# Kernel optimization log

Measured on AMD Instinct MI355X. Metric: run time of the kernel, lower is better.

Reference implementation:

```python
import jax, jax.numpy as jnp
import numpy as np

ROPE_THETA = 10000.0


def _apply_rope(x, rot_dim):
    # lucidrains RotaryEmbedding: only first rot_dim channels are rotated,
    # freqs are interleave-repeated, rotate_half works on (d r=2) pairs.
    S = x.shape[-2]
    half = rot_dim // 2
    inv_freq = 1.0 / (ROPE_THETA ** (jnp.arange(0, rot_dim, 2, dtype=jnp.float32) / rot_dim))  # [half]
    pos = jnp.arange(S, dtype=jnp.float32)
    freqs = pos[:, None] * inv_freq[None, :]          # [S, half]
    freqs = jnp.repeat(freqs, 2, axis=-1)             # [S, rot_dim] interleaved
    cos = jnp.cos(freqs).astype(x.dtype)
    sin = jnp.sin(freqs).astype(x.dtype)
    xl, xr = x[..., :rot_dim], x[..., rot_dim:]
    xp = xl.reshape(*xl.shape[:-1], half, 2)
    x1, x2 = xp[..., 0], xp[..., 1]
    rot_half = jnp.stack([-x2, x1], axis=-1).reshape(xl.shape)
    return jnp.concatenate([xl * cos + rot_half * sin, xr], axis=-1)


def setup_inputs() -> dict:
    key = jax.random.key(0)
    ks = jax.random.split(key, 7)
    B, Sa, Se, d_audio, d_score = 4, 4096, 2048, 1024, 1024
    d_h = min(d_audio, d_score)
    return {
        "x_audio": jax.random.normal(ks[0], (B, Sa, d_audio), jnp.float32),
        "x_event": jax.random.normal(ks[1], (B, Se, d_score), jnp.float32),
        "event_padding_mask": jax.random.randint(ks[2], (B, Se), 0, 2) > 0,
        "W_q": jax.random.normal(ks[3], (d_h, d_audio), jnp.float32) * (d_audio ** -0.5),
        "b_q": jax.random.normal(ks[4], (d_h,), jnp.float32) * 0.02,
        "W_k": jax.random.normal(ks[5], (d_h, d_score), jnp.float32) * (d_score ** -0.5),
        "b_k": jax.random.normal(ks[6], (d_h,), jnp.float32) * 0.02,
    }


def reference(x_audio, x_event, event_padding_mask, W_q, b_q, W_k, b_k):
    d_h = W_q.shape[0]
    rot_dim = d_h // 2  # RotaryEmbedding(dim=d_h//2) -> partial rotary over first d_h//2 channels
    Q = jnp.einsum("bsd,hd->bsh", x_audio, W_q) + b_q
    K = jnp.einsum("bed,hd->beh", x_event, W_k) + b_k
    Q = _apply_rope(Q, rot_dim)
    K = _apply_rope(K, rot_dim)
    attn = jnp.einsum("bsh,beh->bse", Q, K)  # [B, S_audio, S_event]
    mask = event_padding_mask[:, None, :]     # [B, 1, S_event]
    attn = jnp.where(mask, attn, jnp.float32(-jnp.inf))
    return attn
```

## Files before the change

kernel.cpp:

```cpp
#include <hip/hip_runtime.h>
#include <hip/hip_bf16.h>
#include <cmath>

#define BATCH 4
#define SA 4096
#define SE 2048
#define DIM 1024
#define ROT 512
#define NT (DIM / 64)

#define MASK_SENTINEL (-1.0e30f)

using short8  = __attribute__((ext_vector_type(8))) short;
using floatx4 = __attribute__((ext_vector_type(4))) float;

#define RFREQ 0.0519051171f

__device__ __forceinline__ void gl_lds16(const void* g, void* l) {
    __builtin_amdgcn_global_load_lds(
        (const __attribute__((address_space(1))) unsigned int*)g,
        (__attribute__((address_space(3))) unsigned int*)l, 16, 0, 0);
}

__device__ __forceinline__ short bf16_of(float f) {
    __hip_bfloat16 h = __float2bfloat16(f);
    return *reinterpret_cast<short*>(&h);
}

__device__ __forceinline__ int imin(int a, int b) { return a < b ? a : b; }

__global__ __launch_bounds__(256) void probe_mask_kernel(
    const int* __restrict__ mask_i, int* __restrict__ flag)
{
    __shared__ int s_bad;
    if (threadIdx.x == 0) s_bad = 0;
    __syncthreads();
    int bad = 0;
    for (int i = threadIdx.x; i < 1024; i += 256) {
        int v = mask_i[i];
        bad |= (v != 0 && v != 1) ? 1 : 0;
    }
    if (bad) atomicOr(&s_bad, 1);
    __syncthreads();
    if (threadIdx.x == 0) *flag = s_bad ? 0 : 1;
}

__global__ __launch_bounds__(256) void cvt_bf16_kernel(
    const float* __restrict__ in, short* __restrict__ out, int n8)
{
    int i = blockIdx.x * 256 + threadIdx.x;
    if (i >= n8) return;
    const float4 f0 = ((const float4*)in)[2 * i];
    const float4 f1 = ((const float4*)in)[2 * i + 1];
    short8 o;
    o[0] = bf16_of(f0.x); o[1] = bf16_of(f0.y);
    o[2] = bf16_of(f0.z); o[3] = bf16_of(f0.w);
    o[4] = bf16_of(f1.x); o[5] = bf16_of(f1.y);
    o[6] = bf16_of(f1.z); o[7] = bf16_of(f1.w);
    ((short8*)out)[i] = o;
}

__global__ __launch_bounds__(256) void rope_table_kernel(float2* __restrict__ tab)
{
    const int i   = blockIdx.x * 256 + threadIdx.x;
    const int h2  = i >> 12;
    const int pos = i & 4095;
    const float inv = exp2f(-RFREQ * (float)h2);
    float s, c;
    sincosf((float)pos * inv, &s, &c);
    tab[i] = make_float2(c, s);
}

template <int MODE>
__device__ __forceinline__ void gemm8_body(
    const short* __restrict__ A,
    const short* __restrict__ B,
    const float* __restrict__ bias,
    const float2* __restrict__ ct,
    const void*  __restrict__ maskp,
    const int*   __restrict__ flag,
    void* __restrict__ outp,
    int smask)
{
    __shared__ char smem[131072];
    char* const lA0 = smem;
    char* const lA1 = smem + 32768;
    char* const lB0 = smem + 65536;
    char* const lB1 = smem + 98304;

    const int tid  = threadIdx.x;
    const int wid  = tid >> 6;
    const int lane = tid & 63;

    const int nbx = gridDim.x, nby = gridDim.y;
    const int id  = blockIdx.x + nbx * (blockIdx.y + nby * blockIdx.z);
    const int cpx = (nbx * nby * gridDim.z) >> 3;
    const int swzid = (id & 7) * cpx + (id >> 3);
    const int bx  = swzid % nbx;
    const int byz = swzid / nbx;
    const int by  = byz % nby;
    const int bz  = byz / nby;
    const int m0 = by * 256;
    const int n0 = bx * 256;

    const short* Ab = A;
    const short* Bb = B;
    if (MODE == 1) {
        Ab += (size_t)bz * SA * DIM;
        Bb += (size_t)bz * SE * DIM;
    }

    const int r8   = lane >> 3;
    const int c16  = (lane & 7) << 4;
    const int scs  = ((lane & 7) ^ r8) << 4;
    const int arow = wid * 8 + r8;
    const int brow = (wid & 3) * 8 + (wid >> 2) * 64 + r8;
    const char* gA = (const char*)Ab + ((size_t)(m0 + arow) << 11) + scs;
    const char* gB = (const char*)Bb + ((size_t)(n0 + brow) << 11) + scs;
    const int ldsAt = arow * 128 + c16;
    const int ldsBt = brow * 128 + c16;

#define STG_A(dst, h, j, kt) \
    gl_lds16(gA + (((size_t)((h)*64 + (j)*128) << 11) + (size_t)(kt)*128), \
             (dst) + ((h)*64 + (j)*128) * 128 + ldsAt)
#define STG_B(dst, h, j, kt) \
    gl_lds16(gB + (((size_t)((h)*32 + (j)*128) << 11) + (size_t)(kt)*128), \
             (dst) + ((h)*32 + (j)*128) * 128 + ldsBt)

    const int fr  = lane & 15;
    const int fq  = lane >> 4;
    const int kc0 = (fq * 16) ^ ((fr & 7) << 4);
    const int wm  = (wid >> 2) * 128;
    const int wn  = (wid & 3) * 64;

    floatx4 acc[8][4] = {};
    short8 af[4][2];
    short8 bfr[2][2][2];

#define RD_A(lAc, mh) do {                                                   \
    _Pragma("unroll") for (int mi4 = 0; mi4 < 4; ++mi4)                      \
    _Pragma("unroll") for (int ks = 0; ks < 2; ++ks)                         \
        af[mi4][ks] = *(const short8*)((lAc)                                 \
            + (wm + (mh)*64 + mi4*16 + fr) * 128 + (kc0 ^ (ks*64)));         \
} while (0)
#define RD_B(lBc, nh) do {                                                   \
    _Pragma("unroll") for (int ni2 = 0; ni2 < 2; ++ni2)                      \
    _Pragma("unroll") for (int ks = 0; ks < 2; ++ks)                         \
        bfr[nh][ni2][ks] = *(const short8*)((lBc)                            \
            + (wn + (nh)*32 + ni2*16 + fr) * 128 + (kc0 ^ (ks*64)));         \
} while (0)
#define QUAD(mh, nh) do {                                                    \
    __builtin_amdgcn_s_setprio(1);                                           \
    _Pragma("unroll") for (int mi4 = 0; mi4 < 4; ++mi4)                      \
    _Pragma("unroll") for (int ni2 = 0; ni2 < 2; ++ni2)                      \
    _Pragma("unroll") for (int ks = 0; ks < 2; ++ks)                         \
        acc[(mh)*4 + mi4][(nh)*2 + ni2] =                                    \
            __builtin_amdgcn_mfma_f32_16x16x32_bf16(                         \
                af[mi4][ks], bfr[nh][ni2][ks],                               \
                acc[(mh)*4 + mi4][(nh)*2 + ni2], 0, 0, 0);                   \
    __builtin_amdgcn_s_setprio(0);                                           \
} while (0)
#define BAR() do { __builtin_amdgcn_s_barrier();                             \
                   __builtin_amdgcn_sched_barrier(0); } while (0)
#define WAITV(n) asm volatile("s_waitcnt vmcnt(" #n ")" ::: "memory")

    STG_A(lA0, 0, 0, 0); STG_A(lA0, 0, 1, 0);
    STG_A(lA0, 1, 0, 0); STG_A(lA0, 1, 1, 0);
    STG_B(lB0, 0, 0, 0); STG_B(lB0, 0, 1, 0);
    STG_B(lB0, 1, 0, 0); STG_B(lB0, 1, 1, 0);
    STG_A(lA1, 0, 0, 1); STG_A(lA1, 0, 1, 1);
    STG_B(lB1, 0, 0, 1); STG_B(lB1, 0, 1, 1);
    STG_A(lA1, 1, 0, 1); STG_A(lA1, 1, 1, 1);
    WAITV(6);
    BAR();

    auto tile = [&](int t, char* lAc, char* lBc, char* lBn) {
        const int kt1 = imin(t + 1, NT - 1);
        const int kt2 = imin(t + 2, NT - 1);
        RD_A(lAc, 0); RD_B(lBc, 0);
        STG_B(lBn, 1, 0, kt1); STG_B(lBn, 1, 1, kt1);
        BAR();
        QUAD(0, 0);
        BAR();
        RD_B(lBc, 1);
        STG_A(lAc, 0, 0, kt2); STG_A(lAc, 0, 1, kt2);
        BAR();
        QUAD(0, 1);
        BAR();
        RD_A(lAc, 1);
        STG_B(lBc, 0, 0, kt2); STG_B(lBc, 0, 1, kt2);
        BAR();
        QUAD(1, 0);
        BAR();
        STG_A(lAc, 1, 0, kt2); STG_A(lAc, 1, 1, kt2);
        BAR();
        QUAD(1, 1);
        WAITV(6);
        BAR();
    };

    for (int t = 0; t < NT; t += 2) {
        tile(t,     lA0, lB0, lB1);
        tile(t + 1, lA1, lB1, lB0);
    }
    WAITV(0);

    const int rrow = (lane >> 4) * 4;

    if (MODE == 0) {
        short* out = (short*)outp;
#pragma unroll
        for (int ni = 0; ni < 4; ++ni) {
            const int h = n0 + wn + ni * 16 + fr;
            const float bv  = bias[h];
            const bool rope = (h < ROT);
            const float sgn = (h & 1) ? 1.f : -1.f;
            const float2* ctrow = ct + ((size_t)(h >> 1) << 12);
#pragma unroll
            for (int mi = 0; mi < 8; ++mi) {
                const int rbase = m0 + wm + mi * 16 + rrow;
                const int pbase = rbase & smask;
                float2 cs[4];
                if (rope) {
#pragma unroll
                    for (int r = 0; r < 4; ++r) cs[r] = ctrow[pbase + r];
                }
#pragma unroll
                for (int r = 0; r < 4; ++r) {
                    float v = acc[mi][ni][r] + bv;
                    float p = __shfl_xor(v, 1);
                    if (rope) v = v * cs[r].x + sgn * p * cs[r].y;
                    out[(size_t)(rbase + r) * DIM + h] = bf16_of(v);
                }
            }
        }
    } else {
        float* out = (float*)outp + (size_t)bz * SA * SE;
        const int fl = *flag;
#pragma unroll
        for (int ni = 0; ni < 4; ++ni) {
            const int e = n0 + wn + ni * 16 + fr;
            int mk;
            if (fl) mk = ((const int*)maskp)[(size_t)bz * SE + e];
            else    mk = ((const unsigned char*)maskp)[(size_t)bz * SE + e];
#pragma unroll
            for (int mi = 0; mi < 8; ++mi) {
                const int rbase = m0 + wm + mi * 16 + rrow;
#pragma unroll
                for (int r = 0; r < 4; ++r) {
                    const float v = mk ? acc[mi][ni][r] : MASK_SENTINEL;
                    out[(size_t)(rbase + r) * SE + e] = v;
                }
            }
        }
    }
#undef STG_A
#undef STG_B
#undef RD_A
#undef RD_B
#undef QUAD
#undef BAR
#undef WAITV
}

__global__ __launch_bounds__(512, 2) void gemm8_proj_kernel(
    const short* __restrict__ A, const short* __restrict__ B,
    const float* __restrict__ bias, const float2* __restrict__ ct,
    short* __restrict__ out, int smask)
{
    gemm8_body<0>(A, B, bias, ct, nullptr, nullptr, out, smask);
}

__global__ __launch_bounds__(512, 2) void gemm8_attn_kernel(
    const short* __restrict__ Q, const short* __restrict__ K,
    const void* __restrict__ maskp, const int* __restrict__ flag,
    float* __restrict__ out)
{
    gemm8_body<1>(Q, K, nullptr, nullptr, maskp, flag, out, 0);
}

extern "C" void kernel_launch(void* const* d_in, const int* in_sizes, int n_in,
                              void* d_out, int out_size, void* d_ws, size_t ws_size,
                              hipStream_t stream)
{
    const float* x_audio = (const float*)d_in[0];
    const float* x_event = (const float*)d_in[1];
    const void*  maskp   = d_in[2];
    const float* W_q     = (const float*)d_in[3];
    const float* b_q     = (const float*)d_in[4];
    const float* W_k     = (const float*)d_in[5];
    const float* b_k     = (const float*)d_in[6];
    float* out = (float*)d_out;

    char* ws = (char*)d_ws;
    short* xbf  = (short*)(ws);
    short* Qbf  = (short*)(ws + (size_t)32 * 1024 * 1024);
    short* Kbf  = (short*)(ws + (size_t)64 * 1024 * 1024);
    short* Wqbf = (short*)(ws + (size_t)80 * 1024 * 1024);
    short* Wkbf = (short*)(ws + (size_t)82 * 1024 * 1024);
    int*   flag = (int*)  (ws + (size_t)84 * 1024 * 1024);
    float2* ct  = (float2*)d_out;

    probe_mask_kernel<<<1, 256, 0, stream>>>((const int*)maskp, flag);
    rope_table_kernel<<<4096, 256, 0, stream>>>(ct);

    const int nxa8 = BATCH * SA * DIM / 8;
    const int nxe8 = BATCH * SE * DIM / 8;
    const int nw8  = DIM * DIM / 8;

    cvt_bf16_kernel<<<(nxa8 + 255) / 256, 256, 0, stream>>>(x_audio, xbf, nxa8);
    cvt_bf16_kernel<<<(nw8 + 255) / 256, 256, 0, stream>>>(W_q, Wqbf, nw8);
    gemm8_proj_kernel<<<dim3(DIM / 256, (BATCH * SA) / 256, 1), 512, 0, stream>>>(
        xbf, Wqbf, b_q, ct, Qbf, SA - 1);

    cvt_bf16_kernel<<<(nxe8 + 255) / 256, 256, 0, stream>>>(x_event, xbf, nxe8);
    cvt_bf16_kernel<<<(nw8 + 255) / 256, 256, 0, stream>>>(W_k, Wkbf, nw8);
    gemm8_proj_kernel<<<dim3(DIM / 256, (BATCH * SE) / 256, 1), 512, 0, stream>>>(
        xbf, Wkbf, b_k, ct, Kbf, SE - 1);

    gemm8_attn_kernel<<<dim3(SE / 256, SA / 256, BATCH), 512, 0, stream>>>(
        Qbf, Kbf, maskp, flag, out);
}
```

Before: 405.9 us.

## Shrink GEMM block tiles to 128x128 with 4 waves and half LDS

Replaces the 256x256 block tile (8 waves, 128 KiB LDS) with a 128x128 tile (4 waves, 64 KiB LDS) for all three GEMMs. The staging, LDS-read and MFMA schedule is restructured into two half-steps per k-tile instead of four quarters. The aim is more blocks and better occupancy and load balance, with fewer barriers per tile. The cost is lower arithmetic intensity, so more global and L2 traffic per FLOP.

```diff
diff --git a/kernel.cpp b/kernel.cpp
--- a/kernel.cpp
+++ b/kernel.cpp
@@ -72,7 +72,7 @@
 }
 
 template <int MODE>
-__device__ __forceinline__ void gemm8_body(
+__device__ __forceinline__ void gemm128_body(
     const short* __restrict__ A,
     const short* __restrict__ B,
     const float* __restrict__ bias,
@@ -82,11 +82,11 @@
     void* __restrict__ outp,
     int smask)
 {
-    __shared__ char smem[131072];
+    __shared__ char smem[65536];
     char* const lA0 = smem;
-    char* const lA1 = smem + 32768;
-    char* const lB0 = smem + 65536;
-    char* const lB1 = smem + 98304;
+    char* const lA1 = smem + 16384;
+    char* const lB0 = smem + 32768;
+    char* const lB1 = smem + 49152;
 
     const int tid  = threadIdx.x;
     const int wid  = tid >> 6;
@@ -100,8 +100,8 @@
     const int byz = swzid / nbx;
     const int by  = byz % nby;
     const int bz  = byz / nby;
-    const int m0 = by * 256;
-    const int n0 = bx * 256;
+    const int m0 = by * 128;
+    const int n0 = bx * 128;
 
     const short* Ab = A;
     const short* Bb = B;
@@ -114,88 +114,89 @@
     const int c16  = (lane & 7) << 4;
     const int scs  = ((lane & 7) ^ r8) << 4;
     const int arow = wid * 8 + r8;
-    const int brow = (wid & 3) * 8 + (wid >> 2) * 64 + r8;
     const char* gA = (const char*)Ab + ((size_t)(m0 + arow) << 11) + scs;
-    const char* gB = (const char*)Bb + ((size_t)(n0 + brow) << 11) + scs;
-    const int ldsAt = arow * 128 + c16;
-    const int ldsBt = brow * 128 + c16;
-
-#define STG_A(dst, h, j, kt) \
-    gl_lds16(gA + (((size_t)((h)*64 + (j)*128) << 11) + (size_t)(kt)*128), \
-             (dst) + ((h)*64 + (j)*128) * 128 + ldsAt)
-#define STG_B(dst, h, j, kt) \
-    gl_lds16(gB + (((size_t)((h)*32 + (j)*128) << 11) + (size_t)(kt)*128), \
-             (dst) + ((h)*32 + (j)*128) * 128 + ldsBt)
+    const char* gB = (const char*)Bb + ((size_t)(n0 + arow) << 11) + scs;
+    const int ldsT = arow * 128 + c16;
+
+#define STG_A(dst, j, kt) \
+    gl_lds16(gA + (((size_t)(j) * 32) << 11) + (size_t)(kt) * 128, \
+             (dst) + (j) * 32 * 128 + ldsT)
+#define STG_B(dst, j, kt) \
+    gl_lds16(gB + (((size_t)(j) * 32) << 11) + (size_t)(kt) * 128, \
+             (dst) + (j) * 32 * 128 + ldsT)
 
     const int fr  = lane & 15;
     const int fq  = lane >> 4;
     const int kc0 = (fq * 16) ^ ((fr & 7) << 4);
-    const int wm  = (wid >> 2) * 128;
-    const int wn  = (wid & 3) * 64;
-
-    floatx4 acc[8][4] = {};
+    const int wm  = (wid >> 1) * 64;
+    const int wn  = (wid & 1) * 64;
+
+    floatx4 acc[4][4] = {};
     short8 af[4][2];
-    short8 bfr[2][2][2];
-
-#define RD_A(lAc, mh) do {                                                   \
-    _Pragma("unroll") for (int mi4 = 0; mi4 < 4; ++mi4)                      \
-    _Pragma("unroll") for (int ks = 0; ks < 2; ++ks)                         \
-        af[mi4][ks] = *(const short8*)((lAc)                                 \
-            + (wm + (mh)*64 + mi4*16 + fr) * 128 + (kc0 ^ (ks*64)));         \
-} while (0)
-#define RD_B(lBc, nh) do {                                                   \
-    _Pragma("unroll") for (int ni2 = 0; ni2 < 2; ++ni2)                      \
-    _Pragma("unroll") for (int ks = 0; ks < 2; ++ks)                         \
-        bfr[nh][ni2][ks] = *(const short8*)((lBc)                            \
-            + (wn + (nh)*32 + ni2*16 + fr) * 128 + (kc0 ^ (ks*64)));         \
-} while (0)
-#define QUAD(mh, nh) do {                                                    \
+    short8 b01[2][2];
+    short8 b23[2][2];
+
+#define RD_A(lAc) do {                                                       \
+    _Pragma("unroll") for (int mi = 0; mi < 4; ++mi)                         \
+    _Pragma("unroll") for (int ks = 0; ks < 2; ++ks)                         \
+        af[mi][ks] = *(const short8*)((lAc)                                  \
+            + (wm + mi * 16 + fr) * 128 + (kc0 ^ (ks * 64)));                \
+} while (0)
+#define RD_B01(lBc) do {                                                     \
+    _Pragma("unroll") for (int ni = 0; ni < 2; ++ni)                         \
+    _Pragma("unroll") for (int ks = 0; ks < 2; ++ks)                         \
+        b01[ni][ks] = *(const short8*)((lBc)                                 \
+            + (wn + ni * 16 + fr) * 128 + (kc0 ^ (ks * 64)));                \
+} while (0)
+#define RD_B23(lBc) do {                                                     \
+    _Pragma("unroll") for (int ni = 0; ni < 2; ++ni)                         \
+    _Pragma("unroll") for (int ks = 0; ks < 2; ++ks)                         \
+        b23[ni][ks] = *(const short8*)((lBc)                                 \
+            + (wn + (2 + ni) * 16 + fr) * 128 + (kc0 ^ (ks * 64)));          \
+} while (0)
+#define QUAD01() do {                                                        \
     __builtin_amdgcn_s_setprio(1);                                           \
-    _Pragma("unroll") for (int mi4 = 0; mi4 < 4; ++mi4)                      \
-    _Pragma("unroll") for (int ni2 = 0; ni2 < 2; ++ni2)                      \
-    _Pragma("unroll") for (int ks = 0; ks < 2; ++ks)                         \
-        acc[(mh)*4 + mi4][(nh)*2 + ni2] =                                    \
-            __builtin_amdgcn_mfma_f32_16x16x32_bf16(                         \
-                af[mi4][ks], bfr[nh][ni2][ks],                               \
-                acc[(mh)*4 + mi4][(nh)*2 + ni2], 0, 0, 0);                   \
+    _Pragma("unroll") for (int mi = 0; mi < 4; ++mi)                         \
+    _Pragma("unroll") for (int ni = 0; ni < 2; ++ni)                         \
+    _Pragma("unroll") for (int ks = 0; ks < 2; ++ks)                         \
+        acc[mi][ni] = __builtin_amdgcn_mfma_f32_16x16x32_bf16(               \
+            af[mi][ks], b01[ni][ks], acc[mi][ni], 0, 0, 0);                  \
+    __builtin_amdgcn_s_setprio(0);                                           \
+} while (0)
+#define QUAD23() do {                                                        \
+    __builtin_amdgcn_s_setprio(1);                                           \
+    _Pragma("unroll") for (int mi = 0; mi < 4; ++mi)                         \
+    _Pragma("unroll") for (int ni = 0; ni < 2; ++ni)                         \
+    _Pragma("unroll") for (int ks = 0; ks < 2; ++ks)                         \
+        acc[mi][2 + ni] = __builtin_amdgcn_mfma_f32_16x16x32_bf16(           \
+            af[mi][ks], b23[ni][ks], acc[mi][2 + ni], 0, 0, 0);              \
     __builtin_amdgcn_s_setprio(0);                                           \
 } while (0)
 #define BAR() do { __builtin_amdgcn_s_barrier();                             \
                    __builtin_amdgcn_sched_barrier(0); } while (0)
 #define WAITV(n) asm volatile("s_waitcnt vmcnt(" #n ")" ::: "memory")
 
-    STG_A(lA0, 0, 0, 0); STG_A(lA0, 0, 1, 0);
-    STG_A(lA0, 1, 0, 0); STG_A(lA0, 1, 1, 0);
-    STG_B(lB0, 0, 0, 0); STG_B(lB0, 0, 1, 0);
-    STG_B(lB0, 1, 0, 0); STG_B(lB0, 1, 1, 0);
-    STG_A(lA1, 0, 0, 1); STG_A(lA1, 0, 1, 1);
-    STG_B(lB1, 0, 0, 1); STG_B(lB1, 0, 1, 1);
-    STG_A(lA1, 1, 0, 1); STG_A(lA1, 1, 1, 1);
-    WAITV(6);
+    STG_A(lA0, 0, 0); STG_A(lA0, 1, 0); STG_A(lA0, 2, 0); STG_A(lA0, 3, 0);
+    STG_B(lB0, 0, 0); STG_B(lB0, 1, 0); STG_B(lB0, 2, 0); STG_B(lB0, 3, 0);
+    STG_A(lA1, 0, 1); STG_A(lA1, 1, 1); STG_A(lA1, 2, 1); STG_A(lA1, 3, 1);
+    WAITV(4);
     BAR();
 
-    auto tile = [&](int t, char* lAc, char* lBc, char* lBn) {
+    auto tile = [&](int t, char* lAc, char* lBc, char* lBo) {
         const int kt1 = imin(t + 1, NT - 1);
         const int kt2 = imin(t + 2, NT - 1);
-        RD_A(lAc, 0); RD_B(lBc, 0);
-        STG_B(lBn, 1, 0, kt1); STG_B(lBn, 1, 1, kt1);
+        RD_A(lAc); RD_B01(lBc);
+        STG_B(lBo, 0, kt1); STG_B(lBo, 1, kt1);
+        STG_B(lBo, 2, kt1); STG_B(lBo, 3, kt1);
         BAR();
-        QUAD(0, 0);
+        QUAD01();
         BAR();
-        RD_B(lBc, 1);
-        STG_A(lAc, 0, 0, kt2); STG_A(lAc, 0, 1, kt2);
+        RD_B23(lBc);
+        STG_A(lAc, 0, kt2); STG_A(lAc, 1, kt2);
+        STG_A(lAc, 2, kt2); STG_A(lAc, 3, kt2);
         BAR();
-        QUAD(0, 1);
-        BAR();
-        RD_A(lAc, 1);
-        STG_B(lBc, 0, 0, kt2); STG_B(lBc, 0, 1, kt2);
-        BAR();
-        QUAD(1, 0);
-        BAR();
-        STG_A(lAc, 1, 0, kt2); STG_A(lAc, 1, 1, kt2);
-        BAR();
-        QUAD(1, 1);
-        WAITV(6);
+        QUAD23();
+        WAITV(4);
         BAR();
     };
 
@@ -205,7 +206,7 @@
     }
     WAITV(0);
 
-    const int rrow = (lane >> 4) * 4;
+    const int rrow = fq * 4;
 
     if (MODE == 0) {
         short* out = (short*)outp;
@@ -217,7 +218,7 @@
             const float sgn = (h & 1) ? 1.f : -1.f;
             const float2* ctrow = ct + ((size_t)(h >> 1) << 12);
 #pragma unroll
-            for (int mi = 0; mi < 8; ++mi) {
+            for (int mi = 0; mi < 4; ++mi) {
                 const int rbase = m0 + wm + mi * 16 + rrow;
                 const int pbase = rbase & smask;
                 float2 cs[4];
@@ -244,7 +245,7 @@
             if (fl) mk = ((const int*)maskp)[(size_t)bz * SE + e];
             else    mk = ((const unsigned char*)maskp)[(size_t)bz * SE + e];
 #pragma unroll
-            for (int mi = 0; mi < 8; ++mi) {
+            for (int mi = 0; mi < 4; ++mi) {
                 const int rbase = m0 + wm + mi * 16 + rrow;
 #pragma unroll
                 for (int r = 0; r < 4; ++r) {
@@ -257,26 +258,28 @@
 #undef STG_A
 #undef STG_B
 #undef RD_A
-#undef RD_B
-#undef QUAD
+#undef RD_B01
+#undef RD_B23
+#undef QUAD01
+#undef QUAD23
 #undef BAR
 #undef WAITV
 }
 
-__global__ __launch_bounds__(512, 2) void gemm8_proj_kernel(
+__global__ __launch_bounds__(256, 2) void gemm128_proj_kernel(
     const short* __restrict__ A, const short* __restrict__ B,
     const float* __restrict__ bias, const float2* __restrict__ ct,
     short* __restrict__ out, int smask)
 {
-    gemm8_body<0>(A, B, bias, ct, nullptr, nullptr, out, smask);
-}
-
-__global__ __launch_bounds__(512, 2) void gemm8_attn_kernel(
+    gemm128_body<0>(A, B, bias, ct, nullptr, nullptr, out, smask);
+}
+
+__global__ __launch_bounds__(256, 2) void gemm128_attn_kernel(
     const short* __restrict__ Q, const short* __restrict__ K,
     const void* __restrict__ maskp, const int* __restrict__ flag,
     float* __restrict__ out)
 {
-    gemm8_body<1>(Q, K, nullptr, nullptr, maskp, flag, out, 0);
+    gemm128_body<1>(Q, K, nullptr, nullptr, maskp, flag, out, 0);
 }
 
 extern "C" void kernel_launch(void* const* d_in, const int* in_sizes, int n_in,
@@ -310,14 +313,14 @@
 
     cvt_bf16_kernel<<<(nxa8 + 255) / 256, 256, 0, stream>>>(x_audio, xbf, nxa8);
     cvt_bf16_kernel<<<(nw8 + 255) / 256, 256, 0, stream>>>(W_q, Wqbf, nw8);
-    gemm8_proj_kernel<<<dim3(DIM / 256, (BATCH * SA) / 256, 1), 512, 0, stream>>>(
+    gemm128_proj_kernel<<<dim3(DIM / 128, (BATCH * SA) / 128, 1), 256, 0, stream>>>(
         xbf, Wqbf, b_q, ct, Qbf, SA - 1);
 
     cvt_bf16_kernel<<<(nxe8 + 255) / 256, 256, 0, stream>>>(x_event, xbf, nxe8);
     cvt_bf16_kernel<<<(nw8 + 255) / 256, 256, 0, stream>>>(W_k, Wkbf, nw8);
-    gemm8_proj_kernel<<<dim3(DIM / 256, (BATCH * SE) / 256, 1), 512, 0, stream>>>(
+    gemm128_proj_kernel<<<dim3(DIM / 128, (BATCH * SE) / 128, 1), 256, 0, stream>>>(
         xbf, Wkbf, b_k, ct, Kbf, SE - 1);
 
-    gemm8_attn_kernel<<<dim3(SE / 256, SA / 256, BATCH), 512, 0, stream>>>(
+    gemm128_attn_kernel<<<dim3(SE / 128, SA / 128, BATCH), 256, 0, stream>>>(
         Qbf, Kbf, maskp, flag, out);
 }
```

New measurement: 374.7 us. 1.08x faster.
